# Kernel tuning notes

Hardware: AMD Instinct MI355X
Metric: run time of the kernel (lower is better)

## Reference

```python
import jax, jax.numpy as jnp
import numpy as np

B, S, D_MODEL = 2, 2048, 2048
H, HKV, HD = 16, 16, 128


def setup_inputs() -> dict:
    key = jax.random.key(0)
    k1, k2, k3, k4, k5 = jax.random.split(key, 5)
    hidden_states = jax.random.normal(k1, (B, S, D_MODEL), dtype=jnp.float32)
    cos = jax.random.uniform(k2, (S, HD), dtype=jnp.float32)
    sin = jax.random.uniform(k3, (S, HD), dtype=jnp.float32)
    W_qkv = jax.random.normal(k4, (D_MODEL, (H + 2 * HKV) * HD), dtype=jnp.float32) * (D_MODEL ** -0.5)
    W_o = jax.random.normal(k5, (H * HD, D_MODEL), dtype=jnp.float32) * ((H * HD) ** -0.5)
    return {"hidden_states": hidden_states, "cos": cos, "sin": sin, "W_qkv": W_qkv, "W_o": W_o}


def _rotate_half(x):
    x1, x2 = jnp.split(x, 2, axis=-1)
    return jnp.concatenate([-x2, x1], axis=-1)


def reference(hidden_states, cos, sin, W_qkv, W_o):
    b, s, _ = hidden_states.shape
    qkv = jnp.einsum('bsd,de->bse', hidden_states, W_qkv)
    qkv = qkv.reshape(b, s, H + 2 * HKV, HD)  # B S (H+2Hkv) D
    q = qkv[:, :, :H]
    k = qkv[:, :, H:H + HKV]
    v = qkv[:, :, H + HKV:]
    # rotary: cos/sin [S, D] broadcast over batch and heads
    c = cos[None, :, None, :]
    sn = sin[None, :, None, :]
    q = q * c + _rotate_half(q) * sn
    k = k * c + _rotate_half(k) * sn
    # B S H D -> B H S D
    q = jnp.transpose(q, (0, 2, 1, 3))
    k = jnp.transpose(k, (0, 2, 1, 3))
    v = jnp.transpose(v, (0, 2, 1, 3))
    scale = HD ** -0.5
    scores = jnp.einsum('bhqd,bhkd->bhqk', q, k) * scale
    attn = jax.nn.softmax(scores.astype(jnp.float32), axis=-1).astype(q.dtype)
    attn = jax.lax.stop_gradient(attn)  # frozen attention pattern (detach)
    out = jnp.einsum('bhqk,bhkd->bhqd', attn, v)
    out = jnp.transpose(out, (0, 2, 1, 3)).reshape(b, s, H * HD)
    return jnp.einsum('bsd,de->bse', out, W_o)
```

## Files before the change

kernel.cpp:

```cpp
#include <hip/hip_runtime.h>

typedef _Float16 f16;
typedef _Float16 half8 __attribute__((ext_vector_type(8)));
typedef _Float16 half4 __attribute__((ext_vector_type(4)));
typedef float f32x4 __attribute__((ext_vector_type(4)));

#define B_ 2
#define S_ 2048
#define DM_ 2048
#define H_ 16
#define HD_ 128
#define EQ_ 6144
#define SCALE_Q 0.08838834764831845f
#define DEFER_THR 8.0f

__device__ __forceinline__ void gload16(const void* g, void* l) {
  __builtin_amdgcn_global_load_lds(
      (const __attribute__((address_space(1))) unsigned int*)g,
      (__attribute__((address_space(3))) unsigned int*)l, 16, 0, 0);
}

__device__ __forceinline__ float red16_max(float x) {
  float t;
  t = __builtin_bit_cast(float, __builtin_amdgcn_mov_dpp(__builtin_bit_cast(int, x), 0xB1, 0xF, 0xF, true));
  x = fmaxf(x, t);
  t = __builtin_bit_cast(float, __builtin_amdgcn_mov_dpp(__builtin_bit_cast(int, x), 0x4E, 0xF, 0xF, true));
  x = fmaxf(x, t);
  t = __builtin_bit_cast(float, __builtin_amdgcn_mov_dpp(__builtin_bit_cast(int, x), 0x141, 0xF, 0xF, true));
  x = fmaxf(x, t);
  t = __builtin_bit_cast(float, __builtin_amdgcn_mov_dpp(__builtin_bit_cast(int, x), 0x140, 0xF, 0xF, true));
  x = fmaxf(x, t);
  return x;
}
__device__ __forceinline__ float red16_sum(float x) {
  float t;
  t = __builtin_bit_cast(float, __builtin_amdgcn_mov_dpp(__builtin_bit_cast(int, x), 0xB1, 0xF, 0xF, true));
  x += t;
  t = __builtin_bit_cast(float, __builtin_amdgcn_mov_dpp(__builtin_bit_cast(int, x), 0x4E, 0xF, 0xF, true));
  x += t;
  t = __builtin_bit_cast(float, __builtin_amdgcn_mov_dpp(__builtin_bit_cast(int, x), 0x141, 0xF, 0xF, true));
  x += t;
  t = __builtin_bit_cast(float, __builtin_amdgcn_mov_dpp(__builtin_bit_cast(int, x), 0x140, 0xF, 0xF, true));
  x += t;
  return x;
}

__global__ void k_cast(const float* __restrict__ in, f16* __restrict__ out, int n4) {
  int i = blockIdx.x * blockDim.x + threadIdx.x;
  int stride = gridDim.x * blockDim.x;
  for (; i < n4; i += stride) {
    float4 v = ((const float4*)in)[i];
    half4 h = { (f16)v.x, (f16)v.y, (f16)v.z, (f16)v.w };
    ((half4*)out)[i] = h;
  }
}

__global__ void k_tcast(const float* __restrict__ in, f16* __restrict__ out, int K, int N) {
  __shared__ float tile[64][65];
  const int t = threadIdx.x;
  const int nb = blockIdx.x * 64, kb = blockIdx.y * 64;
  const int tr = t >> 4, tc4 = (t & 15) * 4;
  #pragma unroll
  for (int i = 0; i < 4; ++i) {
    int k = tr + i * 16;
    float4 v = *(const float4*)&in[(size_t)(kb + k) * N + nb + tc4];
    tile[k][tc4 + 0] = v.x; tile[k][tc4 + 1] = v.y;
    tile[k][tc4 + 2] = v.z; tile[k][tc4 + 3] = v.w;
  }
  __syncthreads();
  #pragma unroll
  for (int i = 0; i < 4; ++i) {
    int n = tr + i * 16;
    half4 h = { (f16)tile[tc4 + 0][n], (f16)tile[tc4 + 1][n],
                (f16)tile[tc4 + 2][n], (f16)tile[tc4 + 3][n] };
    *(half4*)&out[(size_t)(nb + n) * K + kb + tc4] = h;
  }
}

__global__ __launch_bounds__(256, 2) void k_gemm(
    const f16* __restrict__ A, const f16* __restrict__ Bt,
    f16* __restrict__ C16, float* __restrict__ C32,
    int M, int N, int K, int writeF32)
{
  __shared__ __attribute__((aligned(16))) f16 As[128 * 64];
  __shared__ __attribute__((aligned(16))) f16 Bs[128 * 64];
  const int t = threadIdx.x;
  const int lane = t & 63, wave = t >> 6;
  const int lr = lane & 15, hi4 = lane >> 4;
  const int wr = wave >> 1, wc = wave & 1;
  const int row0 = blockIdx.x * 128, col0 = blockIdx.y * 128;

  const int srow = lane >> 3, schunk = lane & 7;
  const f16* gA = &A[(size_t)(row0 + wave * 32 + srow) * K + schunk * 8];
  const f16* gB = &Bt[(size_t)(col0 + wave * 32 + srow) * K + schunk * 8];
  char* asb = (char*)As;
  char* bsb = (char*)Bs;

  f32x4 acc[4][4];
  #pragma unroll
  for (int m = 0; m < 4; ++m)
    #pragma unroll
    for (int n = 0; n < 4; ++n)
      acc[m][n] = (f32x4){0.f, 0.f, 0.f, 0.f};

  const int nk = K >> 6;
  for (int kt = 0; kt < nk; ++kt) {
    __syncthreads();
    #pragma unroll
    for (int i = 0; i < 4; ++i) {
      gload16(gA + (size_t)(i * 8) * K + kt * 64, asb + wave * 4096 + i * 1024);
      gload16(gB + (size_t)(i * 8) * K + kt * 64, bsb + wave * 4096 + i * 1024);
    }
    __syncthreads();
    #pragma unroll
    for (int ks = 0; ks < 2; ++ks) {
      half8 af[4], bf[4];
      #pragma unroll
      for (int m = 0; m < 4; ++m)
        af[m] = *(const half8*)(asb + (wr * 64 + m * 16 + lr) * 128 + ks * 64 + hi4 * 16);
      #pragma unroll
      for (int n = 0; n < 4; ++n)
        bf[n] = *(const half8*)(bsb + (wc * 64 + n * 16 + lr) * 128 + ks * 64 + hi4 * 16);
      #pragma unroll
      for (int m = 0; m < 4; ++m)
        #pragma unroll
        for (int n = 0; n < 4; ++n)
          acc[m][n] = __builtin_amdgcn_mfma_f32_16x16x32_f16(af[m], bf[n], acc[m][n], 0, 0, 0);
    }
  }
  #pragma unroll
  for (int m = 0; m < 4; ++m)
    #pragma unroll
    for (int n = 0; n < 4; ++n)
      #pragma unroll
      for (int j = 0; j < 4; ++j) {
        int row = row0 + wr * 64 + m * 16 + hi4 * 4 + j;
        int col = col0 + wc * 64 + n * 16 + lr;
        if (writeF32) C32[(size_t)row * N + col] = acc[m][n][j];
        else          C16[(size_t)row * N + col] = (f16)acc[m][n][j];
      }
  (void)M;
}

__global__ void k_rope(const f16* __restrict__ qkv, const float* __restrict__ cosb,
                       const float* __restrict__ sinb, f16* __restrict__ Qf, f16* __restrict__ Kf)
{
  const int bx = blockIdx.x;
  const int bs = bx >> 4;
  const int h = (bx & 15) * 2 + (threadIdx.x >> 7);
  const int d = threadIdx.x & 127;
  const int s = bs & (S_ - 1);
  const int b = bs >> 11;
  float x  = (float)qkv[(size_t)bs * EQ_ + h * HD_ + d];
  float xp = (float)qkv[(size_t)bs * EQ_ + h * HD_ + (d ^ 64)];
  float sgn = (d < 64) ? -1.0f : 1.0f;
  float v = x * cosb[s * HD_ + d] + sgn * xp * sinb[s * HD_ + d];
  if (h < H_) {
    v *= SCALE_Q;
    Qf[(((size_t)(b * H_ + h)) * S_ + s) * HD_ + d] = (f16)v;
  } else {
    Kf[(((size_t)(b * H_ + (h - H_))) * S_ + s) * HD_ + d] = (f16)v;
  }
}

__global__ void k_vtrans(const f16* __restrict__ qkv, f16* __restrict__ VT)
{
  __shared__ __attribute__((aligned(16))) f16 tile[128][136];
  const int bx = blockIdx.x;
  const int st = bx & 15, h = (bx >> 4) & 15, b = bx >> 8;
  const int t = threadIdx.x;
  const int sl = t >> 1, dc = (t & 1) * 64;
  const int bs = b * S_ + st * 128 + sl;
  #pragma unroll
  for (int i = 0; i < 8; ++i) {
    half8 v = *(const half8*)&qkv[(size_t)bs * EQ_ + (32 + h) * HD_ + dc + i * 8];
    *(half8*)&tile[sl][dc + i * 8] = v;
  }
  __syncthreads();
  const int dr = t >> 1, scc = (t & 1) * 64;
  #pragma unroll
  for (int i = 0; i < 8; ++i) {
    half8 v;
    #pragma unroll
    for (int j = 0; j < 8; ++j) v[j] = tile[scc + i * 8 + j][dr];
    *(half8*)&VT[(((size_t)(b * H_ + h)) * HD_ + dr) * S_ + st * 128 + scc + i * 8] = v;
  }
}

__global__ __launch_bounds__(256, 2) void k_attn(
    const f16* __restrict__ Qf, const f16* __restrict__ Kf, const f16* __restrict__ VT,
    f16* __restrict__ Oout)
{
  __shared__ __attribute__((aligned(16))) char lds[32768];
  char* Ks = lds;
  char* Vs = lds + 16384;
  const int bx = blockIdx.x;
  const int qt = bx & 15, h = (bx >> 4) & 15, b = bx >> 8;
  const int t = threadIdx.x, lane = t & 63, wave = t >> 6;
  const int lr = lane & 15, hi4 = lane >> 4;
  char* Ps = Ks + wave * 4096;
  const size_t bh = (size_t)(b * H_ + h);
  const int q0 = qt * 128 + wave * 32;

  half8 qf[2][4];
  #pragma unroll
  for (int m = 0; m < 2; ++m)
    #pragma unroll
    for (int ds = 0; ds < 4; ++ds)
      qf[m][ds] = *(const half8*)&Qf[(bh * S_ + q0 + m * 16 + lr) * HD_ + ds * 32 + hi4 * 8];

  f32x4 o[2][8];
  #pragma unroll
  for (int m = 0; m < 2; ++m)
    #pragma unroll
    for (int dc = 0; dc < 8; ++dc) o[m][dc] = (f32x4){0.f, 0.f, 0.f, 0.f};
  float mstate[2][4], lstate[2][4];
  #pragma unroll
  for (int m = 0; m < 2; ++m)
    #pragma unroll
    for (int j = 0; j < 4; ++j) { mstate[m][j] = -1e30f; lstate[m][j] = 0.f; }

  const f16* Kg = &Kf[bh * S_ * HD_];
  const f16* Vg = &VT[bh * HD_ * S_];

  for (int kt = 0; kt < S_ / 64; ++kt) {
    __syncthreads();
    #pragma unroll
    for (int i = 0; i < 4; ++i) {
      int row = wave * 16 + i * 4 + (lane >> 4);
      int ch  = (lane & 15) ^ (row & 7);
      gload16(Kg + (size_t)(kt * 64 + row) * HD_ + ch * 8, Ks + wave * 4096 + i * 1024);
    }
    #pragma unroll
    for (int i = 0; i < 4; ++i) {
      int d  = wave * 32 + i * 8 + (lane >> 3);
      int ch = (lane & 7) ^ (d & 7);
      gload16(Vg + (size_t)d * S_ + kt * 64 + ch * 8, Vs + wave * 4096 + i * 1024);
    }
    __syncthreads();

    f32x4 sc[2][4];
    #pragma unroll
    for (int m = 0; m < 2; ++m)
      #pragma unroll
      for (int n = 0; n < 4; ++n) sc[m][n] = (f32x4){0.f, 0.f, 0.f, 0.f};
    #pragma unroll
    for (int ds = 0; ds < 4; ++ds) {
      half8 kf[4];
      #pragma unroll
      for (int n = 0; n < 4; ++n) {
        int ar = n * 16 + lr;
        kf[n] = *(const half8*)(Ks + ar * 256 + ((((ds * 4 + hi4) ^ (ar & 7))) << 4));
      }
      #pragma unroll
      for (int m = 0; m < 2; ++m)
        #pragma unroll
        for (int n = 0; n < 4; ++n)
          sc[m][n] = __builtin_amdgcn_mfma_f32_16x16x32_f16(qf[m][ds], kf[n], sc[m][n], 0, 0, 0);
    }
    __syncthreads();

    float mx[2][4];
    #pragma unroll
    for (int m = 0; m < 2; ++m)
      #pragma unroll
      for (int j = 0; j < 4; ++j) {
        mx[m][j] = fmaxf(fmaxf(sc[m][0][j], sc[m][1][j]), fmaxf(sc[m][2][j], sc[m][3][j]));
        mx[m][j] = red16_max(mx[m][j]);
      }
    float dmax = -1e30f;
    #pragma unroll
    for (int m = 0; m < 2; ++m)
      #pragma unroll
      for (int j = 0; j < 4; ++j)
        dmax = fmaxf(dmax, mx[m][j] - mstate[m][j]);
    if (__any(dmax > DEFER_THR)) {
      #pragma unroll
      for (int m = 0; m < 2; ++m)
        #pragma unroll
        for (int j = 0; j < 4; ++j) {
          float nm = fmaxf(mstate[m][j], mx[m][j]);
          float corr = __expf(mstate[m][j] - nm);
          mstate[m][j] = nm;
          lstate[m][j] *= corr;
          #pragma unroll
          for (int dc = 0; dc < 8; ++dc) o[m][dc][j] *= corr;
        }
    }
    float rs[2][4];
    #pragma unroll
    for (int m = 0; m < 2; ++m)
      #pragma unroll
      for (int j = 0; j < 4; ++j) rs[m][j] = 0.f;
    #pragma unroll
    for (int m = 0; m < 2; ++m)
      #pragma unroll
      for (int n = 0; n < 4; ++n)
        #pragma unroll
        for (int j = 0; j < 4; ++j) {
          float p = __expf(sc[m][n][j] - mstate[m][j]);
          sc[m][n][j] = p;
          rs[m][j] += p;
        }
    #pragma unroll
    for (int m = 0; m < 2; ++m)
      #pragma unroll
      for (int j = 0; j < 4; ++j)
        lstate[m][j] += red16_sum(rs[m][j]);

    #pragma unroll
    for (int m = 0; m < 2; ++m)
      #pragma unroll
      for (int n = 0; n < 4; ++n)
        #pragma unroll
        for (int j = 0; j < 4; ++j) {
          int prow = m * 16 + hi4 * 4 + j;
          *(f16*)(Ps + prow * 128 + ((n * 32 + lr * 2) ^ ((prow & 7) << 4))) = (f16)sc[m][n][j];
        }
    asm volatile("" ::: "memory");

    #pragma unroll
    for (int ks = 0; ks < 2; ++ks) {
      half8 pa[2];
      #pragma unroll
      for (int m = 0; m < 2; ++m) {
        int pr = m * 16 + lr;
        pa[m] = *(const half8*)(Ps + pr * 128 + ((((ks * 4 + hi4) ^ (pr & 7))) << 4));
      }
      #pragma unroll
      for (int dc = 0; dc < 8; ++dc) {
        int rv = dc * 16 + lr;
        half8 vb = *(const half8*)(Vs + rv * 128 + ((((ks * 4 + hi4) ^ (rv & 7))) << 4));
        #pragma unroll
        for (int m = 0; m < 2; ++m)
          o[m][dc] = __builtin_amdgcn_mfma_f32_16x16x32_f16(pa[m], vb, o[m][dc], 0, 0, 0);
      }
    }
  }

  float inv[2][4];
  #pragma unroll
  for (int m = 0; m < 2; ++m)
    #pragma unroll
    for (int j = 0; j < 4; ++j) inv[m][j] = 1.0f / lstate[m][j];
  #pragma unroll
  for (int m = 0; m < 2; ++m)
    #pragma unroll
    for (int dc = 0; dc < 8; ++dc)
      #pragma unroll
      for (int j = 0; j < 4; ++j) {
        int row = b * S_ + qt * 128 + wave * 32 + m * 16 + hi4 * 4 + j;
        int col = h * 128 + dc * 16 + lr;
        Oout[(size_t)row * DM_ + col] = (f16)(o[m][dc][j] * inv[m][j]);
      }
}

extern "C" void kernel_launch(void* const* d_in, const int* in_sizes, int n_in,
                              void* d_out, int out_size, void* d_ws, size_t ws_size,
                              hipStream_t stream) {
  (void)in_sizes; (void)n_in; (void)out_size; (void)ws_size;
  const float* hidden = (const float*)d_in[0];
  const float* cosb   = (const float*)d_in[1];
  const float* sinb   = (const float*)d_in[2];
  const float* W_qkv  = (const float*)d_in[3];
  const float* W_o    = (const float*)d_in[4];
  float* out = (float*)d_out;

  f16* Ah    = (f16*)d_ws;
  f16* Wqt   = Ah    + (size_t)8388608;
  f16* Wot   = Wqt   + (size_t)12582912;
  f16* qkv16 = Wot   + (size_t)4194304;
  f16* Qf    = qkv16 + (size_t)25165824;
  f16* Kf    = Qf    + (size_t)8388608;
  f16* VT    = Kf    + (size_t)8388608;
  f16* AO    = VT    + (size_t)8388608;

  k_cast<<<2048, 256, 0, stream>>>(hidden, Ah, 2097152);
  k_tcast<<<dim3(EQ_ / 64, 2048 / 64), 256, 0, stream>>>(W_qkv, Wqt, 2048, EQ_);
  k_tcast<<<dim3(2048 / 64, 2048 / 64), 256, 0, stream>>>(W_o, Wot, 2048, 2048);
  k_gemm<<<dim3(32, EQ_ / 128), 256, 0, stream>>>(Ah, Wqt, qkv16, nullptr, 4096, EQ_, 2048, 0);
  k_rope<<<B_ * S_ * 16, 256, 0, stream>>>(qkv16, cosb, sinb, Qf, Kf);
  k_vtrans<<<512, 256, 0, stream>>>(qkv16, VT);
  k_attn<<<512, 256, 0, stream>>>(Qf, Kf, VT, AO);
  k_gemm<<<dim3(32, 16), 256, 0, stream>>>(AO, Wot, nullptr, out, 4096, 2048, 2048, 1);
}
```

Before: 459.6 us.

## Double-buffer and swizzle GEMM LDS tiles; reorder attention blocks and split waits

The projection GEMM now double-buffers its A/B LDS tiles. It prefetches the next k-tile while computing the current one and keeps one barrier per iteration. The LDS layout is XOR-swizzled to reduce bank conflicts on fragment reads. The attention kernel changes block index mapping so consecutive blocks cover different heads and batches of the same query tile. It also replaces the full post-load sync with a partial vmcnt wait plus barrier, so K can be used while V loads are still in flight. The cost is doubled GEMM LDS use, which may limit occupancy, and the attention path must wait for V explicitly before using it.

Result: faster. 433.9 us (-5.6%).

```diff
diff --git a/kernel.cpp b/kernel.cpp
--- a/kernel.cpp
+++ b/kernel.cpp
@@ -82,8 +82,8 @@
     f16* __restrict__ C16, float* __restrict__ C32,
     int M, int N, int K, int writeF32)
 {
-  __shared__ __attribute__((aligned(16))) f16 As[128 * 64];
-  __shared__ __attribute__((aligned(16))) f16 Bs[128 * 64];
+  __shared__ __attribute__((aligned(16))) f16 As[2 * 128 * 64];
+  __shared__ __attribute__((aligned(16))) f16 Bs[2 * 128 * 64];
   const int t = threadIdx.x;
   const int lane = t & 63, wave = t >> 6;
   const int lr = lane & 15, hi4 = lane >> 4;
@@ -91,8 +91,8 @@
   const int row0 = blockIdx.x * 128, col0 = blockIdx.y * 128;
 
   const int srow = lane >> 3, schunk = lane & 7;
-  const f16* gA = &A[(size_t)(row0 + wave * 32 + srow) * K + schunk * 8];
-  const f16* gB = &Bt[(size_t)(col0 + wave * 32 + srow) * K + schunk * 8];
+  const f16* gA = &A[(size_t)(row0 + wave * 32 + srow) * K + ((schunk ^ srow) * 8)];
+  const f16* gB = &Bt[(size_t)(col0 + wave * 32 + srow) * K + ((schunk ^ srow) * 8)];
   char* asb = (char*)As;
   char* bsb = (char*)Bs;
 
@@ -104,29 +104,46 @@
       acc[m][n] = (f32x4){0.f, 0.f, 0.f, 0.f};
 
   const int nk = K >> 6;
+  #pragma unroll
+  for (int i = 0; i < 4; ++i) {
+    gload16(gA + (size_t)(i * 8) * K, asb + wave * 4096 + i * 1024);
+    gload16(gB + (size_t)(i * 8) * K, bsb + wave * 4096 + i * 1024);
+  }
+  __syncthreads();
+
+  int cur = 0;
   for (int kt = 0; kt < nk; ++kt) {
-    __syncthreads();
-    #pragma unroll
-    for (int i = 0; i < 4; ++i) {
-      gload16(gA + (size_t)(i * 8) * K + kt * 64, asb + wave * 4096 + i * 1024);
-      gload16(gB + (size_t)(i * 8) * K + kt * 64, bsb + wave * 4096 + i * 1024);
-    }
-    __syncthreads();
+    if (kt + 1 < nk) {
+      int nb = cur ^ 1;
+      #pragma unroll
+      for (int i = 0; i < 4; ++i) {
+        gload16(gA + (size_t)(i * 8) * K + (kt + 1) * 64, asb + nb * 16384 + wave * 4096 + i * 1024);
+        gload16(gB + (size_t)(i * 8) * K + (kt + 1) * 64, bsb + nb * 16384 + wave * 4096 + i * 1024);
+      }
+    }
+    const char* ab = asb + cur * 16384;
+    const char* bb = bsb + cur * 16384;
     #pragma unroll
     for (int ks = 0; ks < 2; ++ks) {
       half8 af[4], bf[4];
       #pragma unroll
-      for (int m = 0; m < 4; ++m)
-        af[m] = *(const half8*)(asb + (wr * 64 + m * 16 + lr) * 128 + ks * 64 + hi4 * 16);
-      #pragma unroll
-      for (int n = 0; n < 4; ++n)
-        bf[n] = *(const half8*)(bsb + (wc * 64 + n * 16 + lr) * 128 + ks * 64 + hi4 * 16);
+      for (int m = 0; m < 4; ++m) {
+        int ar = wr * 64 + m * 16 + lr;
+        af[m] = *(const half8*)(ab + ar * 128 + (((ks * 4 + hi4) ^ (ar & 7)) << 4));
+      }
+      #pragma unroll
+      for (int n = 0; n < 4; ++n) {
+        int br = wc * 64 + n * 16 + lr;
+        bf[n] = *(const half8*)(bb + br * 128 + (((ks * 4 + hi4) ^ (br & 7)) << 4));
+      }
       #pragma unroll
       for (int m = 0; m < 4; ++m)
         #pragma unroll
         for (int n = 0; n < 4; ++n)
           acc[m][n] = __builtin_amdgcn_mfma_f32_16x16x32_f16(af[m], bf[n], acc[m][n], 0, 0, 0);
     }
+    __syncthreads();
+    cur ^= 1;
   }
   #pragma unroll
   for (int m = 0; m < 4; ++m)
@@ -195,7 +212,8 @@
   char* Ks = lds;
   char* Vs = lds + 16384;
   const int bx = blockIdx.x;
-  const int qt = bx & 15, h = (bx >> 4) & 15, b = bx >> 8;
+  const int hg = bx & 31, qt = bx >> 5;
+  const int h = hg & 15, b = hg >> 4;
   const int t = threadIdx.x, lane = t & 63, wave = t >> 6;
   const int lr = lane & 15, hi4 = lane >> 4;
   char* Ps = Ks + wave * 4096;
@@ -237,7 +255,9 @@
       int ch = (lane & 7) ^ (d & 7);
       gload16(Vg + (size_t)d * S_ + kt * 64 + ch * 8, Vs + wave * 4096 + i * 1024);
     }
-    __syncthreads();
+    asm volatile("s_waitcnt vmcnt(4)" ::: "memory");
+    __builtin_amdgcn_s_barrier();
+    __builtin_amdgcn_sched_barrier(0);
 
     f32x4 sc[2][4];
     #pragma unroll
```
